# Kernel optimization log

Measured on AMD Instinct MI355X. Metric: run time of the kernel, lower is better.

## Reference

```python
import jax, jax.numpy as jnp
import numpy as np

NUM_HEADS = 16
HEAD_DIM = 64
D_MODEL = NUM_HEADS * HEAD_DIM  # 1024
B, L = 512, 64


def setup_inputs() -> dict:
    key = jax.random.key(0)
    ks = jax.random.split(key, 6)
    s = 1.0 / np.sqrt(D_MODEL)
    x = jax.random.normal(ks[0], (B, L, D_MODEL), dtype=jnp.float32)
    bias = jax.random.normal(ks[1], (1, NUM_HEADS, L, L), dtype=jnp.float32)
    Wq = jax.random.normal(ks[2], (D_MODEL, NUM_HEADS * HEAD_DIM), dtype=jnp.float32) * s
    Wk = jax.random.normal(ks[3], (D_MODEL, NUM_HEADS * HEAD_DIM), dtype=jnp.float32) * s
    Wv = jax.random.normal(ks[4], (D_MODEL, NUM_HEADS * HEAD_DIM), dtype=jnp.float32) * s
    Wo = jax.random.normal(ks[5], (NUM_HEADS * HEAD_DIM, D_MODEL), dtype=jnp.float32) * s
    return {"x": x, "bias": bias, "Wq": Wq, "Wk": Wk, "Wv": Wv, "Wo": Wo}


def reference(x, bias, Wq, Wk, Wv, Wo):
    Bsz, Ls, D = x.shape
    H, Dh = NUM_HEADS, HEAD_DIM
    # QKV projections (no bias), reshape to [B, H, L, Dh]
    q = (x @ Wq).reshape(Bsz, Ls, H, Dh).transpose(0, 2, 1, 3)
    k = (x @ Wk).reshape(Bsz, Ls, H, Dh).transpose(0, 2, 1, 3)
    v = (x @ Wv).reshape(Bsz, Ls, H, Dh).transpose(0, 2, 1, 3)
    scale = jnp.sqrt(jnp.float32(Dh))
    # [B, H, L, L]
    attn_logits = jnp.einsum('bhqd,bhkd->bhqk', q, k) / scale + bias
    attn_weights = jax.nn.softmax(attn_logits, axis=-1)
    # weighted sum -> [B, L, H*Dh]
    out = jnp.einsum('bhqk,bhkd->bhqd', attn_weights, v)
    out = out.transpose(0, 2, 1, 3).reshape(Bsz, Ls, H * Dh)
    return out @ Wo
```

## Files before the change

kernel.cpp:

```cpp
#include <hip/hip_runtime.h>
#include <hip/hip_bf16.h>
#include <stdint.h>

__device__ inline float bf2f(ushort u) {
    union { uint32_t u; float f; } v; v.u = ((uint32_t)u) << 16; return v.f;
}
__device__ inline ushort f2bf(float f) {
    union { float f; uint32_t u; } v; v.f = f;
    uint32_t u = v.u;
    uint32_t r = (u + 0x7fffu + ((u >> 16) & 1u)) >> 16;
    return (ushort)r;
}
__device__ inline uint32_t pk2bf(uint32_t flo, uint32_t fhi) {
    uint32_t lo = (flo + 0x7fffu + ((flo >> 16) & 1u)) >> 16;
    uint32_t hi = (fhi + 0x7fffu + ((fhi >> 16) & 1u)) >> 16;
    return lo | (hi << 16);
}

typedef __attribute__((ext_vector_type(8))) short bf16x8;
typedef __attribute__((ext_vector_type(4))) float f32x4;

__device__ inline void gload_lds16(const ushort* g, ushort* l) {
    __builtin_amdgcn_global_load_lds(
        (const __attribute__((address_space(1))) void*)g,
        (__attribute__((address_space(3))) void*)l, 16, 0, 0);
}

__global__ void transpose1024(const float* __restrict__ Wq, const float* __restrict__ Wk,
                              const float* __restrict__ Wv, const float* __restrict__ Wo,
                              ushort* __restrict__ WqT, ushort* __restrict__ WkT,
                              ushort* __restrict__ WvT, ushort* __restrict__ WoT) {
    const float* in; ushort* out;
    switch (blockIdx.z) {
        case 0: in = Wq; out = WqT; break;
        case 1: in = Wk; out = WkT; break;
        case 2: in = Wv; out = WvT; break;
        default: in = Wo; out = WoT; break;
    }
    __shared__ ushort tile[64][65];
    const int t = threadIdx.x;
    const int c = t & 63, rq = t >> 6;
    const int bx = blockIdx.x * 64, by = blockIdx.y * 64;
#pragma unroll
    for (int i = 0; i < 16; ++i) {
        int r = i * 4 + rq;
        tile[r][c] = f2bf(in[(size_t)(by + r) * 1024 + bx + c]);
    }
    __syncthreads();
#pragma unroll
    for (int i = 0; i < 16; ++i) {
        int r = i * 4 + rq;
        out[(size_t)(bx + r) * 1024 + by + c] = tile[c][r];
    }
}

__global__ __launch_bounds__(256)
void cast_bf16(const float* __restrict__ in, ushort* __restrict__ out, size_t n8) {
    size_t i = (size_t)blockIdx.x * blockDim.x + threadIdx.x;
    const size_t stride = (size_t)gridDim.x * blockDim.x;
    for (; i < n8; i += stride) {
        const uint4 lo = *(const uint4*)&in[i * 8];
        const uint4 hi = *(const uint4*)&in[i * 8 + 4];
        uint4 o;
        o.x = pk2bf(lo.x, lo.y); o.y = pk2bf(lo.z, lo.w);
        o.z = pk2bf(hi.x, hi.y); o.w = pk2bf(hi.z, hi.w);
        *(uint4*)&out[i * 8] = o;
    }
}

template <bool C_F32>
__global__ __launch_bounds__(512, 2)
void gemm256(const ushort* __restrict__ A, int lda, const ushort* __restrict__ Bt,
             void* __restrict__ C_, int M, int N, int K) {
    __shared__ __attribute__((aligned(16))) ushort lds[65536];
    const int t = threadIdx.x;
    const int lane = t & 63, wave = t >> 6;
    const int wm = wave >> 2, wn = wave & 3;
    const int quad = lane >> 4, l16 = lane & 15;

    const int gx = N >> 8;
    const int nwg = gridDim.x * gridDim.y;
    int wg = blockIdx.y * gridDim.x + blockIdx.x;
    {
        const int q = nwg >> 3, r = nwg & 7;
        const int xcd = wg & 7, loc = wg >> 3;
        wg = (xcd < r ? xcd * (q + 1) : r * (q + 1) + (xcd - r) * q) + loc;
    }
    const int m0 = (wg / gx) << 8, n0 = (wg % gx) << 8;

    const f32x4 zero = {0.f, 0.f, 0.f, 0.f};
    f32x4 acc[8][4];
#pragma unroll
    for (int i = 0; i < 8; ++i)
#pragma unroll
        for (int j = 0; j < 4; ++j) acc[i][j] = zero;

    auto STAGE = [&](const ushort* __restrict__ src, int ldb, int rc0, int kcol,
                     int regio, int buf) {
        ushort* l = &lds[buf * 32768 + regio];
#pragma unroll
        for (int j = 0; j < 2; ++j) {
            const int g = j * 512 + t;
            const int r = g >> 2;
            const int cg = (((g & 3) ^ ((r >> 1) & 3)) * 8);
            gload_lds16(&src[(size_t)(rc0 + r) * ldb + kcol + cg],
                        &l[(j * 512 + wave * 64) * 8]);
        }
    };
    auto LOFF = [&](int R) { return R * 32 + (quad ^ ((R >> 1) & 3)) * 8; };

    const int NT = K >> 6;
    STAGE(A, lda, m0, 0, 0, 0);
    STAGE(Bt, K, n0, 0, 16384, 0);
    STAGE(A, lda, m0, 32, 8192, 0);
    STAGE(Bt, K, n0, 32, 24576, 0);
    asm volatile("s_waitcnt vmcnt(4)" ::: "memory");
    __builtin_amdgcn_s_barrier();

    int cur = 0;
    for (int kt = 0; kt < NT; ++kt) {
        const bool nx = kt + 1 < NT;
        const int kn = (kt + 1) << 6;
        const ushort* la0 = &lds[cur * 32768];
        const ushort* lb0 = &lds[cur * 32768 + 16384];
        const ushort* la1 = la0 + 8192;
        const ushort* lb1 = lb0 + 8192;
        bf16x8 af[4], bf[4];

#pragma unroll
        for (int i = 0; i < 4; ++i) {
            af[i] = *(const bf16x8*)&la0[LOFF(wm * 128 + i * 16 + l16)];
            bf[i] = *(const bf16x8*)&lb0[LOFF(wn * 64 + i * 16 + l16)];
        }
        if (nx) STAGE(A, lda, m0, kn, 0, cur ^ 1);
        __builtin_amdgcn_s_barrier();
        __builtin_amdgcn_s_setprio(1);
#pragma unroll
        for (int i = 0; i < 4; ++i)
#pragma unroll
            for (int n = 0; n < 4; ++n)
                acc[i][n] = __builtin_amdgcn_mfma_f32_16x16x32_bf16(af[i], bf[n], acc[i][n], 0, 0, 0);
        __builtin_amdgcn_s_setprio(0);
        __builtin_amdgcn_s_barrier();

#pragma unroll
        for (int i = 0; i < 4; ++i)
            af[i] = *(const bf16x8*)&la0[LOFF(wm * 128 + (i + 4) * 16 + l16)];
        if (nx) STAGE(Bt, K, n0, kn, 16384, cur ^ 1);
        __builtin_amdgcn_s_barrier();
        __builtin_amdgcn_s_setprio(1);
#pragma unroll
        for (int i = 0; i < 4; ++i)
#pragma unroll
            for (int n = 0; n < 4; ++n)
                acc[i + 4][n] = __builtin_amdgcn_mfma_f32_16x16x32_bf16(af[i], bf[n], acc[i + 4][n], 0, 0, 0);
        __builtin_amdgcn_s_setprio(0);
        if (nx) asm volatile("s_waitcnt vmcnt(4)" ::: "memory");
        else    asm volatile("s_waitcnt vmcnt(0)" ::: "memory");
        __builtin_amdgcn_s_barrier();

#pragma unroll
        for (int i = 0; i < 4; ++i) {
            af[i] = *(const bf16x8*)&la1[LOFF(wm * 128 + i * 16 + l16)];
            bf[i] = *(const bf16x8*)&lb1[LOFF(wn * 64 + i * 16 + l16)];
        }
        if (nx) STAGE(A, lda, m0, kn + 32, 8192, cur ^ 1);
        __builtin_amdgcn_s_barrier();
        __builtin_amdgcn_s_setprio(1);
#pragma unroll
        for (int i = 0; i < 4; ++i)
#pragma unroll
            for (int n = 0; n < 4; ++n)
                acc[i][n] = __builtin_amdgcn_mfma_f32_16x16x32_bf16(af[i], bf[n], acc[i][n], 0, 0, 0);
        __builtin_amdgcn_s_setprio(0);
        __builtin_amdgcn_s_barrier();

#pragma unroll
        for (int i = 0; i < 4; ++i)
            af[i] = *(const bf16x8*)&la1[LOFF(wm * 128 + (i + 4) * 16 + l16)];
        if (nx) STAGE(Bt, K, n0, kn + 32, 24576, cur ^ 1);
        __builtin_amdgcn_s_barrier();
        __builtin_amdgcn_s_setprio(1);
#pragma unroll
        for (int i = 0; i < 4; ++i)
#pragma unroll
            for (int n = 0; n < 4; ++n)
                acc[i + 4][n] = __builtin_amdgcn_mfma_f32_16x16x32_bf16(af[i], bf[n], acc[i + 4][n], 0, 0, 0);
        __builtin_amdgcn_s_setprio(0);
        if (nx) asm volatile("s_waitcnt vmcnt(4)" ::: "memory");
        __builtin_amdgcn_s_barrier();

        cur ^= 1;
    }

#pragma unroll
    for (int mt = 0; mt < 8; ++mt)
#pragma unroll
        for (int nt = 0; nt < 4; ++nt)
#pragma unroll
            for (int r4 = 0; r4 < 4; ++r4) {
                const int row = m0 + wm * 128 + mt * 16 + quad * 4 + r4;
                const int col = n0 + wn * 64 + nt * 16 + l16;
                if (C_F32) ((float*)C_)[(size_t)row * N + col] = acc[mt][nt][r4];
                else       ((ushort*)C_)[(size_t)row * N + col] = f2bf(acc[mt][nt][r4]);
            }
}

__global__ __launch_bounds__(256)
void attn_mfma(ushort* __restrict__ QK, const ushort* __restrict__ Vt,
               const float* __restrict__ bias, int CROWS) {
    const int t = threadIdx.x;
    const int lane = t & 63, wave = t >> 6;
    const int quad = lane >> 4, l16 = lane & 15;
    const int b = blockIdx.x >> 4, h = blockIdx.x & 15;
    const int SQK = 2048;
    const size_t qbase = (size_t)b * 64 * SQK + (size_t)h * 64;
    const size_t kbase = qbase + 1024;
    const size_t vbase = (size_t)(h * 64) * CROWS + (size_t)b * 64;

    __shared__ __attribute__((aligned(16))) ushort Pl[4 * 16 * 72];

    bf16x8 qf[2];
#pragma unroll
    for (int ks = 0; ks < 2; ++ks)
        qf[ks] = *(const bf16x8*)&QK[qbase + (size_t)(wave * 16 + l16) * SQK + ks * 32 + quad * 8];

    const f32x4 zero = {0.f, 0.f, 0.f, 0.f};
    f32x4 s[4];
#pragma unroll
    for (int nt = 0; nt < 4; ++nt) s[nt] = zero;
#pragma unroll
    for (int nt = 0; nt < 4; ++nt)
#pragma unroll
        for (int ks = 0; ks < 2; ++ks) {
            bf16x8 kf = *(const bf16x8*)&QK[kbase + (size_t)(nt * 16 + l16) * SQK + ks * 32 + quad * 8];
            s[nt] = __builtin_amdgcn_mfma_f32_16x16x32_bf16(qf[ks], kf, s[nt], 0, 0, 0);
        }

    const int q0 = wave * 16 + quad * 4;
    float p[4][4];
#pragma unroll
    for (int nt = 0; nt < 4; ++nt)
#pragma unroll
        for (int r4 = 0; r4 < 4; ++r4)
            p[nt][r4] = s[nt][r4] * 0.125f +
                        bias[(size_t)(h * 64 + q0 + r4) * 64 + nt * 16 + l16];

    float rinv[4];
#pragma unroll
    for (int r4 = 0; r4 < 4; ++r4) {
        float m = fmaxf(fmaxf(p[0][r4], p[1][r4]), fmaxf(p[2][r4], p[3][r4]));
        m = fmaxf(m, __shfl_xor(m, 1));
        m = fmaxf(m, __shfl_xor(m, 2));
        m = fmaxf(m, __shfl_xor(m, 4));
        m = fmaxf(m, __shfl_xor(m, 8));
#pragma unroll
        for (int nt = 0; nt < 4; ++nt) p[nt][r4] = __expf(p[nt][r4] - m);
        float sum = p[0][r4] + p[1][r4] + p[2][r4] + p[3][r4];
        sum += __shfl_xor(sum, 1);
        sum += __shfl_xor(sum, 2);
        sum += __shfl_xor(sum, 4);
        sum += __shfl_xor(sum, 8);
        rinv[r4] = 1.f / sum;
    }

#pragma unroll
    for (int nt = 0; nt < 4; ++nt)
#pragma unroll
        for (int r4 = 0; r4 < 4; ++r4)
            Pl[(wave * 16 + quad * 4 + r4) * 72 + nt * 16 + l16] = f2bf(p[nt][r4]);
    __syncthreads();

    bf16x8 pa[2];
#pragma unroll
    for (int ks = 0; ks < 2; ++ks)
        pa[ks] = *(const bf16x8*)&Pl[(wave * 16 + l16) * 72 + ks * 32 + quad * 8];
    f32x4 o[4];
#pragma unroll
    for (int nt = 0; nt < 4; ++nt) o[nt] = zero;
#pragma unroll
    for (int nt = 0; nt < 4; ++nt)
#pragma unroll
        for (int ks = 0; ks < 2; ++ks) {
            bf16x8 vf = *(const bf16x8*)&Vt[vbase + (size_t)(nt * 16 + l16) * CROWS + ks * 32 + quad * 8];
            o[nt] = __builtin_amdgcn_mfma_f32_16x16x32_bf16(pa[ks], vf, o[nt], 0, 0, 0);
        }

#pragma unroll
    for (int nt = 0; nt < 4; ++nt)
#pragma unroll
        for (int r4 = 0; r4 < 4; ++r4)
            QK[qbase + (size_t)(q0 + r4) * SQK + nt * 16 + l16] = f2bf(o[nt][r4] * rinv[r4]);
}

extern "C" void kernel_launch(void* const* d_in, const int* in_sizes, int n_in,
                              void* d_out, int out_size, void* d_ws, size_t ws_size,
                              hipStream_t stream) {
    const float* x    = (const float*)d_in[0];
    const float* bias = (const float*)d_in[1];
    const float* Wq   = (const float*)d_in[2];
    const float* Wk   = (const float*)d_in[3];
    const float* Wv   = (const float*)d_in[4];
    const float* Wo   = (const float*)d_in[5];
    float* out = (float*)d_out;

    const size_t D = 1024;
    const size_t WB = 4 * D * D * 2;

    int CHUNK_B = 128;
    if (ws_size >= WB + (size_t)512 * 64 * 6144)      CHUNK_B = 512;
    else if (ws_size >= WB + (size_t)256 * 64 * 6144) CHUNK_B = 256;
    const int NCHUNK = 512 / CHUNK_B;
    const size_t CROWS = (size_t)CHUNK_B * 64;
    const size_t CELEM = CROWS * D;

    ushort* WqT = (ushort*)d_ws;
    ushort* WkT = WqT + D * D;
    ushort* WvT = WkT + D * D;
    ushort* WoT = WvT + D * D;
    ushort* QKc = WoT + D * D;
    ushort* Vtc = QKc + CROWS * 2048;

    transpose1024<<<dim3(16, 16, 4), 256, 0, stream>>>(Wq, Wk, Wv, Wo, WqT, WkT, WvT, WoT);

    for (int c = 0; c < NCHUNK; ++c) {
        const float* xc = x + (size_t)c * CELEM;
        float* outc = out + (size_t)c * CELEM;
        ushort* Xc = (ushort*)outc;
        cast_bf16<<<2048, 256, 0, stream>>>(xc, Xc, CELEM / 8);
        gemm256<false><<<dim3(8, CROWS / 256), 512, 0, stream>>>(
            Xc, 1024, WqT, QKc, (int)CROWS, 2048, 1024);
        gemm256<false><<<dim3(CROWS / 256, 4), 512, 0, stream>>>(
            WvT, 1024, Xc, Vtc, 1024, (int)CROWS, 1024);
        attn_mfma<<<CHUNK_B * 16, 256, 0, stream>>>(QKc, Vtc, bias, (int)CROWS);
        gemm256<true><<<dim3(4, CROWS / 256), 512, 0, stream>>>(
            QKc, 2048, WoT, outc, (int)CROWS, 1024, 1024);
    }
}
```

Measured before the change: 610.5 us.

## Restage GEMM LDS tiles as 128-row by 64-column blocks with 8-way XOR swizzle

```diff
diff --git a/kernel.cpp b/kernel.cpp
--- a/kernel.cpp
+++ b/kernel.cpp
@@ -101,39 +101,45 @@
 #pragma unroll
         for (int j = 0; j < 2; ++j) {
             const int g = j * 512 + t;
-            const int r = g >> 2;
-            const int cg = (((g & 3) ^ ((r >> 1) & 3)) * 8);
+            const int r = g >> 3;
+            const int cg = (((g & 7) ^ (r & 7)) * 8);
             gload_lds16(&src[(size_t)(rc0 + r) * ldb + kcol + cg],
                         &l[(j * 512 + wave * 64) * 8]);
         }
     };
-    auto LOFF = [&](int R) { return R * 32 + (quad ^ ((R >> 1) & 3)) * 8; };
+    auto LOFF = [&](int R, int gq) { return R * 64 + ((gq ^ (R & 7)) * 8); };
 
     const int NT = K >> 6;
+    const int abase = wm * 8192;
+    const int bbase = 16384 + (wn >> 1) * 8192;
+    const int brow = (wn & 1) * 64;
+
     STAGE(A, lda, m0, 0, 0, 0);
+    STAGE(A, lda, m0 + 128, 0, 8192, 0);
     STAGE(Bt, K, n0, 0, 16384, 0);
-    STAGE(A, lda, m0, 32, 8192, 0);
-    STAGE(Bt, K, n0, 32, 24576, 0);
-    asm volatile("s_waitcnt vmcnt(4)" ::: "memory");
+    STAGE(Bt, K, n0 + 128, 0, 24576, 0);
+    asm volatile("s_waitcnt vmcnt(0)" ::: "memory");
     __builtin_amdgcn_s_barrier();
 
     int cur = 0;
     for (int kt = 0; kt < NT; ++kt) {
         const bool nx = kt + 1 < NT;
         const int kn = (kt + 1) << 6;
-        const ushort* la0 = &lds[cur * 32768];
-        const ushort* lb0 = &lds[cur * 32768 + 16384];
-        const ushort* la1 = la0 + 8192;
-        const ushort* lb1 = lb0 + 8192;
+        const ushort* la = &lds[cur * 32768 + abase];
+        const ushort* lb = &lds[cur * 32768 + bbase];
         bf16x8 af[4], bf[4];
 
+        if (nx) STAGE(A, lda, m0, kn, 0, cur ^ 1);
+        if (kt > 0) {
+            if (nx) asm volatile("s_waitcnt vmcnt(2)" ::: "memory");
+            else    asm volatile("s_waitcnt vmcnt(0)" ::: "memory");
+        }
+        __builtin_amdgcn_s_barrier();
 #pragma unroll
         for (int i = 0; i < 4; ++i) {
-            af[i] = *(const bf16x8*)&la0[LOFF(wm * 128 + i * 16 + l16)];
-            bf[i] = *(const bf16x8*)&lb0[LOFF(wn * 64 + i * 16 + l16)];
-        }
-        if (nx) STAGE(A, lda, m0, kn, 0, cur ^ 1);
-        __builtin_amdgcn_s_barrier();
+            af[i] = *(const bf16x8*)&la[LOFF(i * 16 + l16, quad)];
+            bf[i] = *(const bf16x8*)&lb[LOFF(brow + i * 16 + l16, quad)];
+        }
         __builtin_amdgcn_s_setprio(1);
 #pragma unroll
         for (int i = 0; i < 4; ++i)
@@ -145,8 +151,8 @@
 
 #pragma unroll
         for (int i = 0; i < 4; ++i)
-            af[i] = *(const bf16x8*)&la0[LOFF(wm * 128 + (i + 4) * 16 + l16)];
-        if (nx) STAGE(Bt, K, n0, kn, 16384, cur ^ 1);
+            af[i] = *(const bf16x8*)&la[LOFF((i + 4) * 16 + l16, quad)];
+        if (nx) STAGE(A, lda, m0 + 128, kn, 8192, cur ^ 1);
         __builtin_amdgcn_s_barrier();
         __builtin_amdgcn_s_setprio(1);
 #pragma unroll
@@ -155,16 +161,14 @@
             for (int n = 0; n < 4; ++n)
                 acc[i + 4][n] = __builtin_amdgcn_mfma_f32_16x16x32_bf16(af[i], bf[n], acc[i + 4][n], 0, 0, 0);
         __builtin_amdgcn_s_setprio(0);
-        if (nx) asm volatile("s_waitcnt vmcnt(4)" ::: "memory");
-        else    asm volatile("s_waitcnt vmcnt(0)" ::: "memory");
         __builtin_amdgcn_s_barrier();
 
 #pragma unroll
         for (int i = 0; i < 4; ++i) {
-            af[i] = *(const bf16x8*)&la1[LOFF(wm * 128 + i * 16 + l16)];
-            bf[i] = *(const bf16x8*)&lb1[LOFF(wn * 64 + i * 16 + l16)];
-        }
-        if (nx) STAGE(A, lda, m0, kn + 32, 8192, cur ^ 1);
+            af[i] = *(const bf16x8*)&la[LOFF(i * 16 + l16, 4 + quad)];
+            bf[i] = *(const bf16x8*)&lb[LOFF(brow + i * 16 + l16, 4 + quad)];
+        }
+        if (nx) STAGE(Bt, K, n0, kn, 16384, cur ^ 1);
         __builtin_amdgcn_s_barrier();
         __builtin_amdgcn_s_setprio(1);
 #pragma unroll
@@ -177,8 +181,8 @@
 
 #pragma unroll
         for (int i = 0; i < 4; ++i)
-            af[i] = *(const bf16x8*)&la1[LOFF(wm * 128 + (i + 4) * 16 + l16)];
-        if (nx) STAGE(Bt, K, n0, kn + 32, 24576, cur ^ 1);
+            af[i] = *(const bf16x8*)&la[LOFF((i + 4) * 16 + l16, 4 + quad)];
+        if (nx) STAGE(Bt, K, n0 + 128, kn, 24576, cur ^ 1);
         __builtin_amdgcn_s_barrier();
         __builtin_amdgcn_s_setprio(1);
 #pragma unroll
@@ -187,7 +191,6 @@
             for (int n = 0; n < 4; ++n)
                 acc[i + 4][n] = __builtin_amdgcn_mfma_f32_16x16x32_bf16(af[i], bf[n], acc[i + 4][n], 0, 0, 0);
         __builtin_amdgcn_s_setprio(0);
-        if (nx) asm volatile("s_waitcnt vmcnt(4)" ::: "memory");
         __builtin_amdgcn_s_barrier();
 
         cur ^= 1;
```

Measured after the change: 607.0 us. No clear change (-0.6%).
